# Optimization experiments

Measured on AMD Instinct MI355X. Metric: run time of the kernel, lower is better.

## Reference

```python
import jax, jax.numpy as jnp
import numpy as np

B, S = 8, 8192        # batch of texts, chars per text
D = 64                # char_emb_size = (64, 64)
V = 96                # len(valid_chars) + 1


def setup_inputs() -> dict:
    key = jax.random.key(0)
    k_ids, k_emb = jax.random.split(key)
    # tokenized text: indices into valid_chars (always < V-1, matching .index())
    text_ids = jax.random.randint(k_ids, (B, S), 0, V - 1).astype(jnp.int32)
    # frozen embedding table, row i -> flattened D x D matrix
    emb = jax.random.normal(k_emb, (V, D * D), dtype=jnp.float32)
    return {"text_ids": text_ids, "emb": emb}


def reference(text_ids, emb):
    b, s = text_ids.shape
    d = int(np.sqrt(emb.shape[1]))
    table = emb.reshape(-1, d, d)                      # [V, D, D]
    # context_vec starts as identity (torch.eye(max(emb_size)))
    ctx0 = jnp.broadcast_to(jnp.eye(d, dtype=emb.dtype), (b, d, d))

    def step(ctx, ids_t):
        # ids_t: [B] char ids at this timestep
        E = table[ids_t]                               # [B, D, D] gather
        ctx = jnp.cos(jnp.einsum('bij,bjk->bik', ctx, E))
        return ctx, None

    ctx, _ = jax.lax.scan(step, ctx0, text_ids.T)      # scan over S
    return ctx                                         # [B, D, D]
```

## Files before the change

kernel.cpp:

```cpp
#include <hip/hip_runtime.h>


#define BB 8
#define SS 8192
#define DD 64

__device__ __forceinline__ float host_cosf(float y)
{
#pragma clang fp contract(off)
    const double hpi_inv = 0x1.45F306DC9C883p+23;
    const double hpi     = 0x1.921FB54442D18p0;
    const double c0 = 0x1p0;
    const double c1 = -0x1.ffffffd0c621cp-2;
    const double c2 = 0x1.55553e1068f19p-5;
    const double c3 = -0x1.6c087e89a359dp-10;
    const double c4 = 0x1.99343027bf8c3p-16;
    const double s1 = -0x1.555545995a603p-3;
    const double s2 = 0x1.1107605230bc4p-7;
    const double s3 = -0x1.994eb3774cf24p-13;

    const double x = (double)y;
    double r  = x * hpi_inv;
    int    n  = (((int)r) + 0x800000) >> 24;
    double xr = fma(-(double)n, hpi, x);

    const int  mm   = (n + 1) & 3;
    const double s  = (mm == 1 || mm == 2) ? -1.0 : 1.0;
    const bool negt = (mm & 2) != 0;

    double x2  = xr * xr;
    double x4  = x2 * x2;
    double cc2 = fma(x2, c4, c3);
    double cc1 = fma(x2, c1, c0);
    double x6  = x4 * x2;
    double cp  = fma(x4, c2, cc1);
    float fcos = (float)fma(x6, cc2, cp);
    fcos = negt ? -fcos : fcos;

    double xs  = xr * s;
    double x3  = xs * x2;
    double sp1 = fma(x2, s3, s2);
    double x7  = x3 * x2;
    double sr  = fma(x3, s1, xs);
    float fsin = (float)fma(x7, sp1, sr);

    return (n & 1) ? fsin : fcos;
}

__global__ void transpose_kernel(const float* __restrict__ emb,
                                 float* __restrict__ embT)
{
    const int id = blockIdx.x;
    const int t  = threadIdx.x;
    const float* src = emb + (size_t)id * (DD * DD);
    float*       dst = embT + (size_t)id * (DD * DD);
#pragma unroll
    for (int kk = 0; kk < 16; ++kk) {
        const int lin = kk * 256 + t;
        const int j = lin >> 6, c = lin & 63;
        dst[(j >> 2) * 256 + c * 4 + (j & 3)] = src[lin];
    }
}

#define ROX(S,J)   "v_readlane_b32 s" #S ", %[vr], " #J "\n\t"
#define FRX(S,E,J) "v_fmac_f32 %[acc], s" #S ", v" #E "\n\t" \
                   "v_readlane_b32 s" #S ", %[vr], " #J "\n\t"
#define FOX(S,E)   "v_fmac_f32 %[acc], s" #S ", v" #E "\n\t"
#define WQ         "s_waitcnt vmcnt(15)\n\t"
#define LDQ(D0,D3,VO,OFF) \
    "global_load_dwordx4 v[" #D0 ":" #D3 "], " VO ", s[46:47] offset:" OFF "\n\t"

__global__ __launch_bounds__(64, 1)
void text2vec_kernel(const int* __restrict__ ids,
                     const float* __restrict__ emb,
                     const float* __restrict__ embT,
                     float* __restrict__ out)
{
    const int blk  = blockIdx.x;
    const int b    = blk & 7;
    const int r    = blk >> 3;
    const int lane = threadIdx.x;

    const int* bids = ids + b * SS;
    const uintptr_t ta = (uintptr_t)embT;
    const unsigned tlo = (unsigned)ta, thi = (unsigned)(ta >> 32);
    unsigned vo0 = (unsigned)lane * 16u;
    unsigned vo1 = vo0 + 4096u, vo2 = vo0 + 8192u, vo3 = vo0 + 12288u;

    const int id0 = bids[0], id1 = bids[1], id2 = bids[2];

    float acc  = emb[(size_t)(unsigned)id0 * (DD * DD) + r * DD + lane];
    float vrow = 0.0f;

    const double d_hpinv = 0x1.45F306DC9C883p+23;
    const double d_hpi   = 0x1.921FB54442D18p0;
    const double d_c0 = 0x1p0;
    const double d_c1 = -0x1.ffffffd0c621cp-2;
    const double d_c2 = 0x1.55553e1068f19p-5;
    const double d_c3 = -0x1.6c087e89a359dp-10;
    const double d_c4 = 0x1.99343027bf8c3p-16;
    const double d_s1 = -0x1.555545995a603p-3;
    const double d_s2 = 0x1.1107605230bc4p-7;
    const double d_s3 = -0x1.994eb3774cf24p-13;

    asm volatile(
        "s_lshl_b32 s44, %[id1], 14\n\t"
        "s_add_u32 s46, %[tlo], s44\n\t"
        "s_addc_u32 s47, %[thi], 0\n\t"
        LDQ(64,67,"%[vo0]","0")    LDQ(68,71,"%[vo0]","1024")
        LDQ(72,75,"%[vo0]","2048") LDQ(76,79,"%[vo0]","3072")
        LDQ(80,83,"%[vo1]","0")    LDQ(84,87,"%[vo1]","1024")
        LDQ(88,91,"%[vo1]","2048") LDQ(92,95,"%[vo1]","3072")
        LDQ(96,99,"%[vo2]","0")    LDQ(100,103,"%[vo2]","1024")
        LDQ(104,107,"%[vo2]","2048") LDQ(108,111,"%[vo2]","3072")
        LDQ(112,115,"%[vo3]","0")  LDQ(116,119,"%[vo3]","1024")
        LDQ(120,123,"%[vo3]","2048") LDQ(124,127,"%[vo3]","3072")
        "s_mov_b32 s41, %[id2]\n\t"
        "s_mov_b32 s40, 1\n\t"

        "T2V_LOOP:\n\t"
        "v_cvt_f64_f32 v[8:9], %[acc]\n\t"
        "v_mul_f64 v[10:11], v[8:9], %[hpinv]\n\t"
        "v_cvt_i32_f64 v12, v[10:11]\n\t"
        "v_add_u32 v12, 0x800000, v12\n\t"
        "v_ashrrev_i32 v12, 24, v12\n\t"
        "v_cvt_f64_i32 v[10:11], v12\n\t"
        "v_fma_f64 v[8:9], -v[10:11], %[hpi], v[8:9]\n\t"
        "v_add_u32 v13, 1, v12\n\t"
        "v_and_b32 v14, 2, v13\n\t"
        "v_cmp_ne_u32 s[56:57], 0, v14\n\t"
        "v_and_b32 v14, 3, v13\n\t"
        "v_add_u32 v14, 1, v14\n\t"
        "v_and_b32 v14, 2, v14\n\t"
        "v_cmp_ne_u32 vcc, 0, v14\n\t"
        "v_mov_b32 v14, 0x3ff00000\n\t"
        "v_mov_b32 v15, 0xbff00000\n\t"
        "v_cndmask_b32 v15, v14, v15, vcc\n\t"
        "v_mov_b32 v14, 0\n\t"
        "v_mul_f64 v[16:17], v[8:9], v[8:9]\n\t"
        "v_mul_f64 v[18:19], v[16:17], v[16:17]\n\t"
        "v_fma_f64 v[20:21], v[16:17], %[c4], %[c3]\n\t"
        "v_fma_f64 v[22:23], v[16:17], %[c1], %[c0]\n\t"
        "v_mul_f64 v[24:25], v[18:19], v[16:17]\n\t"
        "v_fma_f64 v[22:23], v[18:19], %[c2], v[22:23]\n\t"
        "v_fma_f64 v[20:21], v[24:25], v[20:21], v[22:23]\n\t"
        "v_cvt_f32_f64 v26, v[20:21]\n\t"
        "v_xor_b32 v27, 0x80000000, v26\n\t"
        "v_cndmask_b32 v26, v26, v27, s[56:57]\n\t"
        "v_mul_f64 v[18:19], v[8:9], v[14:15]\n\t"
        "v_mul_f64 v[20:21], v[18:19], v[16:17]\n\t"
        "v_fma_f64 v[22:23], v[16:17], %[s3], %[s2]\n\t"
        "v_mul_f64 v[24:25], v[20:21], v[16:17]\n\t"
        "v_fma_f64 v[18:19], v[20:21], %[s1], v[18:19]\n\t"
        "v_fma_f64 v[18:19], v[24:25], v[22:23], v[18:19]\n\t"
        "v_cvt_f32_f64 v27, v[18:19]\n\t"
        "v_and_b32 v14, 1, v12\n\t"
        "v_cmp_ne_u32 vcc, 0, v14\n\t"
        "v_cndmask_b32 %[vr], v26, v27, vcc\n\t"
        "v_mov_b32 %[acc], 0\n\t"
        "s_waitcnt lgkmcnt(0)\n\t"
        "s_lshl_b32 s44, s41, 14\n\t"
        "s_add_u32 s46, %[tlo], s44\n\t"
        "s_addc_u32 s47, %[thi], 0\n\t"
        "s_add_u32 s43, s40, 2\n\t"
        "s_and_b32 s43, s43, 8191\n\t"
        "s_lshl_b32 s43, s43, 2\n\t"
        "s_load_dword s41, %[bids], s43\n\t"
        ROX(50,0) ROX(51,1) ROX(52,2) ROX(53,3) ROX(54,4) ROX(55,5)
        WQ FRX(50,64,6)   FRX(51,65,7)   FRX(52,66,8)   FRX(53,67,9)   LDQ(64,67,"%[vo0]","0")
        WQ FRX(54,68,10)  FRX(55,69,11)  FRX(50,70,12)  FRX(51,71,13)  LDQ(68,71,"%[vo0]","1024")
        WQ FRX(52,72,14)  FRX(53,73,15)  FRX(54,74,16)  FRX(55,75,17)  LDQ(72,75,"%[vo0]","2048")
        WQ FRX(50,76,18)  FRX(51,77,19)  FRX(52,78,20)  FRX(53,79,21)  LDQ(76,79,"%[vo0]","3072")
        WQ FRX(54,80,22)  FRX(55,81,23)  FRX(50,82,24)  FRX(51,83,25)  LDQ(80,83,"%[vo1]","0")
        WQ FRX(52,84,26)  FRX(53,85,27)  FRX(54,86,28)  FRX(55,87,29)  LDQ(84,87,"%[vo1]","1024")
        WQ FRX(50,88,30)  FRX(51,89,31)  FRX(52,90,32)  FRX(53,91,33)  LDQ(88,91,"%[vo1]","2048")
        WQ FRX(54,92,34)  FRX(55,93,35)  FRX(50,94,36)  FRX(51,95,37)  LDQ(92,95,"%[vo1]","3072")
        WQ FRX(52,96,38)  FRX(53,97,39)  FRX(54,98,40)  FRX(55,99,41)  LDQ(96,99,"%[vo2]","0")
        WQ FRX(50,100,42) FRX(51,101,43) FRX(52,102,44) FRX(53,103,45) LDQ(100,103,"%[vo2]","1024")
        WQ FRX(54,104,46) FRX(55,105,47) FRX(50,106,48) FRX(51,107,49) LDQ(104,107,"%[vo2]","2048")
        WQ FRX(52,108,50) FRX(53,109,51) FRX(54,110,52) FRX(55,111,53) LDQ(108,111,"%[vo2]","3072")
        WQ FRX(50,112,54) FRX(51,113,55) FRX(52,114,56) FRX(53,115,57) LDQ(112,115,"%[vo3]","0")
        WQ FRX(54,116,58) FRX(55,117,59) FRX(50,118,60) FRX(51,119,61) LDQ(116,119,"%[vo3]","1024")
        WQ FRX(52,120,62) FRX(53,121,63) FOX(54,122)    FOX(55,123)    LDQ(120,123,"%[vo3]","2048")
        WQ FOX(50,124)    FOX(51,125)    FOX(52,126)    FOX(53,127)    LDQ(124,127,"%[vo3]","3072")
        "s_addk_i32 s40, 1\n\t"
        "s_cmpk_lt_i32 s40, 0x2000\n\t"
        "s_cbranch_scc1 T2V_LOOP\n\t"
        "s_waitcnt vmcnt(0) lgkmcnt(0)\n\t"
        : [acc] "+v"(acc), [vr] "+v"(vrow)
        : [tlo] "s"(tlo), [thi] "s"(thi), [bids] "s"(bids),
          [vo0] "v"(vo0), [vo1] "v"(vo1), [vo2] "v"(vo2), [vo3] "v"(vo3),
          [id1] "s"(id1), [id2] "s"(id2),
          [hpinv] "s"(d_hpinv), [hpi] "s"(d_hpi), [c4] "s"(d_c4),
          [c1] "s"(d_c1), [c2] "s"(d_c2), [s1] "s"(d_s1), [s3] "s"(d_s3),
          [c3] "v"(d_c3), [c0] "v"(d_c0), [s2] "v"(d_s2)
        : "memory", "scc", "vcc",
          "s40","s41","s42","s43","s44","s45","s46","s47",
          "s50","s51","s52","s53","s54","s55","s56","s57",
          "v8","v9","v10","v11","v12","v13","v14","v15","v16","v17",
          "v18","v19","v20","v21","v22","v23","v24","v25","v26","v27",
          "v64","v65","v66","v67","v68","v69","v70","v71",
          "v72","v73","v74","v75","v76","v77","v78","v79",
          "v80","v81","v82","v83","v84","v85","v86","v87",
          "v88","v89","v90","v91","v92","v93","v94","v95",
          "v96","v97","v98","v99","v100","v101","v102","v103",
          "v104","v105","v106","v107","v108","v109","v110","v111",
          "v112","v113","v114","v115","v116","v117","v118","v119",
          "v120","v121","v122","v123","v124","v125","v126","v127");

    vrow = host_cosf(acc);
    out[b * (DD * DD) + r * DD + lane] = vrow;
}

extern "C" void kernel_launch(void* const* d_in, const int* in_sizes, int n_in,
                              void* d_out, int out_size, void* d_ws, size_t ws_size,
                              hipStream_t stream)
{
    const int*   ids = (const int*)  d_in[0];
    const float* emb = (const float*)d_in[1];
    float*       out = (float*)      d_out;
    float*       embT = (float*)     d_ws;

    const int V = in_sizes[1] / (DD * DD);

    transpose_kernel<<<dim3(V), dim3(256), 0, stream>>>(emb, embT);
    text2vec_kernel<<<dim3(BB * DD), dim3(DD), 0, stream>>>(ids, emb, embT, out);
}
```

Measured before the change: 3.708 ms.

## Compute two context rows per wavefront to reuse each streamed embedding load

Each 64-lane block now owns two rows of the context matrix instead of one. Every embedding-matrix column it streams from global memory feeds two FMA chains, and the two cosine evaluations are interleaved for ILP. The grid is halved, so block count and global/L2 load traffic per step both drop. The cost is more serial VALU and readlane work per wave on a latency-bound recurrence, fewer waves to spread across CUs, and more clobbered SGPRs.

```diff
diff --git a/kernel.cpp b/kernel.cpp
--- a/kernel.cpp
+++ b/kernel.cpp
@@ -62,10 +62,12 @@
     }
 }
 
-#define ROX(S,J)   "v_readlane_b32 s" #S ", %[vr], " #J "\n\t"
-#define FRX(S,E,J) "v_fmac_f32 %[acc], s" #S ", v" #E "\n\t" \
-                   "v_readlane_b32 s" #S ", %[vr], " #J "\n\t"
-#define FOX(S,E)   "v_fmac_f32 %[acc], s" #S ", v" #E "\n\t"
+#define RLA(S,J)   "v_readlane_b32 s" #S ", %[vra], " #J "\n\t"
+#define RLB(S,J)   "v_readlane_b32 s" #S ", %[vrb], " #J "\n\t"
+#define FMA_(S,E)  "v_fmac_f32 %[aca], s" #S ", v" #E "\n\t"
+#define FMB_(S,E)  "v_fmac_f32 %[acb], s" #S ", v" #E "\n\t"
+#define DSLOT(SA,SB,E,J)  FMA_(SA,E) FMB_(SB,E) RLA(SA,J) RLB(SB,J)
+#define DSLOTN(SA,SB,E)   FMA_(SA,E) FMB_(SB,E)
 #define WQ         "s_waitcnt vmcnt(15)\n\t"
 #define LDQ(D0,D3,VO,OFF) \
     "global_load_dwordx4 v[" #D0 ":" #D3 "], " VO ", s[46:47] offset:" OFF "\n\t"
@@ -78,7 +80,8 @@
 {
     const int blk  = blockIdx.x;
     const int b    = blk & 7;
-    const int r    = blk >> 3;
+    const int rp   = blk >> 3;
+    const int r0   = rp * 2, r1 = rp * 2 + 1;
     const int lane = threadIdx.x;
 
     const int* bids = ids + b * SS;
@@ -89,8 +92,9 @@
 
     const int id0 = bids[0], id1 = bids[1], id2 = bids[2];
 
-    float acc  = emb[(size_t)(unsigned)id0 * (DD * DD) + r * DD + lane];
-    float vrow = 0.0f;
+    float aca = emb[(size_t)(unsigned)id0 * (DD * DD) + r0 * DD + lane];
+    float acb = emb[(size_t)(unsigned)id0 * (DD * DD) + r1 * DD + lane];
+    float vra = 0.0f, vrb = 0.0f;
 
     const double d_hpinv = 0x1.45F306DC9C883p+23;
     const double d_hpi   = 0x1.921FB54442D18p0;
@@ -119,45 +123,84 @@
         "s_mov_b32 s40, 1\n\t"
 
         "T2V_LOOP:\n\t"
-        "v_cvt_f64_f32 v[8:9], %[acc]\n\t"
+        "v_cvt_f64_f32 v[8:9], %[aca]\n\t"
+        "v_cvt_f64_f32 v[28:29], %[acb]\n\t"
         "v_mul_f64 v[10:11], v[8:9], %[hpinv]\n\t"
+        "v_mul_f64 v[30:31], v[28:29], %[hpinv]\n\t"
         "v_cvt_i32_f64 v12, v[10:11]\n\t"
+        "v_cvt_i32_f64 v32, v[30:31]\n\t"
         "v_add_u32 v12, 0x800000, v12\n\t"
+        "v_add_u32 v32, 0x800000, v32\n\t"
         "v_ashrrev_i32 v12, 24, v12\n\t"
+        "v_ashrrev_i32 v32, 24, v32\n\t"
         "v_cvt_f64_i32 v[10:11], v12\n\t"
+        "v_cvt_f64_i32 v[30:31], v32\n\t"
         "v_fma_f64 v[8:9], -v[10:11], %[hpi], v[8:9]\n\t"
+        "v_fma_f64 v[28:29], -v[30:31], %[hpi], v[28:29]\n\t"
         "v_add_u32 v13, 1, v12\n\t"
+        "v_add_u32 v33, 1, v32\n\t"
         "v_and_b32 v14, 2, v13\n\t"
+        "v_and_b32 v34, 2, v33\n\t"
         "v_cmp_ne_u32 s[56:57], 0, v14\n\t"
+        "v_cmp_ne_u32 s[58:59], 0, v34\n\t"
         "v_and_b32 v14, 3, v13\n\t"
+        "v_and_b32 v34, 3, v33\n\t"
         "v_add_u32 v14, 1, v14\n\t"
+        "v_add_u32 v34, 1, v34\n\t"
         "v_and_b32 v14, 2, v14\n\t"
-        "v_cmp_ne_u32 vcc, 0, v14\n\t"
+        "v_and_b32 v34, 2, v34\n\t"
+        "v_cmp_ne_u32 s[36:37], 0, v14\n\t"
+        "v_cmp_ne_u32 s[38:39], 0, v34\n\t"
         "v_mov_b32 v14, 0x3ff00000\n\t"
         "v_mov_b32 v15, 0xbff00000\n\t"
-        "v_cndmask_b32 v15, v14, v15, vcc\n\t"
+        "v_cndmask_b32 v15, v14, v15, s[36:37]\n\t"
+        "v_mov_b32 v34, 0x3ff00000\n\t"
+        "v_mov_b32 v35, 0xbff00000\n\t"
+        "v_cndmask_b32 v35, v34, v35, s[38:39]\n\t"
         "v_mov_b32 v14, 0\n\t"
+        "v_mov_b32 v34, 0\n\t"
         "v_mul_f64 v[16:17], v[8:9], v[8:9]\n\t"
+        "v_mul_f64 v[36:37], v[28:29], v[28:29]\n\t"
         "v_mul_f64 v[18:19], v[16:17], v[16:17]\n\t"
+        "v_mul_f64 v[38:39], v[36:37], v[36:37]\n\t"
         "v_fma_f64 v[20:21], v[16:17], %[c4], %[c3]\n\t"
+        "v_fma_f64 v[40:41], v[36:37], %[c4], %[c3]\n\t"
         "v_fma_f64 v[22:23], v[16:17], %[c1], %[c0]\n\t"
+        "v_fma_f64 v[42:43], v[36:37], %[c1], %[c0]\n\t"
         "v_mul_f64 v[24:25], v[18:19], v[16:17]\n\t"
+        "v_mul_f64 v[44:45], v[38:39], v[36:37]\n\t"
         "v_fma_f64 v[22:23], v[18:19], %[c2], v[22:23]\n\t"
+        "v_fma_f64 v[42:43], v[38:39], %[c2], v[42:43]\n\t"
         "v_fma_f64 v[20:21], v[24:25], v[20:21], v[22:23]\n\t"
+        "v_fma_f64 v[40:41], v[44:45], v[40:41], v[42:43]\n\t"
         "v_cvt_f32_f64 v26, v[20:21]\n\t"
+        "v_cvt_f32_f64 v46, v[40:41]\n\t"
         "v_xor_b32 v27, 0x80000000, v26\n\t"
+        "v_xor_b32 v47, 0x80000000, v46\n\t"
         "v_cndmask_b32 v26, v26, v27, s[56:57]\n\t"
+        "v_cndmask_b32 v46, v46, v47, s[58:59]\n\t"
         "v_mul_f64 v[18:19], v[8:9], v[14:15]\n\t"
+        "v_mul_f64 v[38:39], v[28:29], v[34:35]\n\t"
         "v_mul_f64 v[20:21], v[18:19], v[16:17]\n\t"
+        "v_mul_f64 v[40:41], v[38:39], v[36:37]\n\t"
         "v_fma_f64 v[22:23], v[16:17], %[s3], %[s2]\n\t"
+        "v_fma_f64 v[42:43], v[36:37], %[s3], %[s2]\n\t"
         "v_mul_f64 v[24:25], v[20:21], v[16:17]\n\t"
+        "v_mul_f64 v[44:45], v[40:41], v[36:37]\n\t"
         "v_fma_f64 v[18:19], v[20:21], %[s1], v[18:19]\n\t"
+        "v_fma_f64 v[38:39], v[40:41], %[s1], v[38:39]\n\t"
         "v_fma_f64 v[18:19], v[24:25], v[22:23], v[18:19]\n\t"
+        "v_fma_f64 v[38:39], v[44:45], v[42:43], v[38:39]\n\t"
         "v_cvt_f32_f64 v27, v[18:19]\n\t"
+        "v_cvt_f32_f64 v47, v[38:39]\n\t"
         "v_and_b32 v14, 1, v12\n\t"
-        "v_cmp_ne_u32 vcc, 0, v14\n\t"
-        "v_cndmask_b32 %[vr], v26, v27, vcc\n\t"
-        "v_mov_b32 %[acc], 0\n\t"
+        "v_and_b32 v34, 1, v32\n\t"
+        "v_cmp_ne_u32 s[30:31], 0, v14\n\t"
+        "v_cmp_ne_u32 s[32:33], 0, v34\n\t"
+        "v_cndmask_b32 %[vra], v26, v27, s[30:31]\n\t"
+        "v_cndmask_b32 %[vrb], v46, v47, s[32:33]\n\t"
+        "v_mov_b32 %[aca], 0\n\t"
+        "v_mov_b32 %[acb], 0\n\t"
         "s_waitcnt lgkmcnt(0)\n\t"
         "s_lshl_b32 s44, s41, 14\n\t"
         "s_add_u32 s46, %[tlo], s44\n\t"
@@ -166,28 +209,29 @@
         "s_and_b32 s43, s43, 8191\n\t"
         "s_lshl_b32 s43, s43, 2\n\t"
         "s_load_dword s41, %[bids], s43\n\t"
-        ROX(50,0) ROX(51,1) ROX(52,2) ROX(53,3) ROX(54,4) ROX(55,5)
-        WQ FRX(50,64,6)   FRX(51,65,7)   FRX(52,66,8)   FRX(53,67,9)   LDQ(64,67,"%[vo0]","0")
-        WQ FRX(54,68,10)  FRX(55,69,11)  FRX(50,70,12)  FRX(51,71,13)  LDQ(68,71,"%[vo0]","1024")
-        WQ FRX(52,72,14)  FRX(53,73,15)  FRX(54,74,16)  FRX(55,75,17)  LDQ(72,75,"%[vo0]","2048")
-        WQ FRX(50,76,18)  FRX(51,77,19)  FRX(52,78,20)  FRX(53,79,21)  LDQ(76,79,"%[vo0]","3072")
-        WQ FRX(54,80,22)  FRX(55,81,23)  FRX(50,82,24)  FRX(51,83,25)  LDQ(80,83,"%[vo1]","0")
-        WQ FRX(52,84,26)  FRX(53,85,27)  FRX(54,86,28)  FRX(55,87,29)  LDQ(84,87,"%[vo1]","1024")
-        WQ FRX(50,88,30)  FRX(51,89,31)  FRX(52,90,32)  FRX(53,91,33)  LDQ(88,91,"%[vo1]","2048")
-        WQ FRX(54,92,34)  FRX(55,93,35)  FRX(50,94,36)  FRX(51,95,37)  LDQ(92,95,"%[vo1]","3072")
-        WQ FRX(52,96,38)  FRX(53,97,39)  FRX(54,98,40)  FRX(55,99,41)  LDQ(96,99,"%[vo2]","0")
-        WQ FRX(50,100,42) FRX(51,101,43) FRX(52,102,44) FRX(53,103,45) LDQ(100,103,"%[vo2]","1024")
-        WQ FRX(54,104,46) FRX(55,105,47) FRX(50,106,48) FRX(51,107,49) LDQ(104,107,"%[vo2]","2048")
-        WQ FRX(52,108,50) FRX(53,109,51) FRX(54,110,52) FRX(55,111,53) LDQ(108,111,"%[vo2]","3072")
-        WQ FRX(50,112,54) FRX(51,113,55) FRX(52,114,56) FRX(53,115,57) LDQ(112,115,"%[vo3]","0")
-        WQ FRX(54,116,58) FRX(55,117,59) FRX(50,118,60) FRX(51,119,61) LDQ(116,119,"%[vo3]","1024")
-        WQ FRX(52,120,62) FRX(53,121,63) FOX(54,122)    FOX(55,123)    LDQ(120,123,"%[vo3]","2048")
-        WQ FOX(50,124)    FOX(51,125)    FOX(52,126)    FOX(53,127)    LDQ(124,127,"%[vo3]","3072")
+        RLA(50,0) RLB(60,0) RLA(51,1) RLB(61,1) RLA(52,2) RLB(62,2)
+        RLA(53,3) RLB(63,3) RLA(54,4) RLB(64,4) RLA(55,5) RLB(65,5)
+        WQ DSLOT(50,60,64,6)   DSLOT(51,61,65,7)   DSLOT(52,62,66,8)   DSLOT(53,63,67,9)   LDQ(64,67,"%[vo0]","0")
+        WQ DSLOT(54,64,68,10)  DSLOT(55,65,69,11)  DSLOT(50,60,70,12)  DSLOT(51,61,71,13)  LDQ(68,71,"%[vo0]","1024")
+        WQ DSLOT(52,62,72,14)  DSLOT(53,63,73,15)  DSLOT(54,64,74,16)  DSLOT(55,65,75,17)  LDQ(72,75,"%[vo0]","2048")
+        WQ DSLOT(50,60,76,18)  DSLOT(51,61,77,19)  DSLOT(52,62,78,20)  DSLOT(53,63,79,21)  LDQ(76,79,"%[vo0]","3072")
+        WQ DSLOT(54,64,80,22)  DSLOT(55,65,81,23)  DSLOT(50,60,82,24)  DSLOT(51,61,83,25)  LDQ(80,83,"%[vo1]","0")
+        WQ DSLOT(52,62,84,26)  DSLOT(53,63,85,27)  DSLOT(54,64,86,28)  DSLOT(55,65,87,29)  LDQ(84,87,"%[vo1]","1024")
+        WQ DSLOT(50,60,88,30)  DSLOT(51,61,89,31)  DSLOT(52,62,90,32)  DSLOT(53,63,91,33)  LDQ(88,91,"%[vo1]","2048")
+        WQ DSLOT(54,64,92,34)  DSLOT(55,65,93,35)  DSLOT(50,60,94,36)  DSLOT(51,61,95,37)  LDQ(92,95,"%[vo1]","3072")
+        WQ DSLOT(52,62,96,38)  DSLOT(53,63,97,39)  DSLOT(54,64,98,40)  DSLOT(55,65,99,41)  LDQ(96,99,"%[vo2]","0")
+        WQ DSLOT(50,60,100,42) DSLOT(51,61,101,43) DSLOT(52,62,102,44) DSLOT(53,63,103,45) LDQ(100,103,"%[vo2]","1024")
+        WQ DSLOT(54,64,104,46) DSLOT(55,65,105,47) DSLOT(50,60,106,48) DSLOT(51,61,107,49) LDQ(104,107,"%[vo2]","2048")
+        WQ DSLOT(52,62,108,50) DSLOT(53,63,109,51) DSLOT(54,64,110,52) DSLOT(55,65,111,53) LDQ(108,111,"%[vo2]","3072")
+        WQ DSLOT(50,60,112,54) DSLOT(51,61,113,55) DSLOT(52,62,114,56) DSLOT(53,63,115,57) LDQ(112,115,"%[vo3]","0")
+        WQ DSLOT(54,64,116,58) DSLOT(55,65,117,59) DSLOT(50,60,118,60) DSLOT(51,61,119,61) LDQ(116,119,"%[vo3]","1024")
+        WQ DSLOT(52,62,120,62) DSLOT(53,63,121,63) DSLOTN(54,64,122)   DSLOTN(55,65,123)   LDQ(120,123,"%[vo3]","2048")
+        WQ DSLOTN(50,60,124)   DSLOTN(51,61,125)   DSLOTN(52,62,126)   DSLOTN(53,63,127)   LDQ(124,127,"%[vo3]","3072")
         "s_addk_i32 s40, 1\n\t"
         "s_cmpk_lt_i32 s40, 0x2000\n\t"
         "s_cbranch_scc1 T2V_LOOP\n\t"
         "s_waitcnt vmcnt(0) lgkmcnt(0)\n\t"
-        : [acc] "+v"(acc), [vr] "+v"(vrow)
+        : [aca] "+v"(aca), [acb] "+v"(acb), [vra] "+v"(vra), [vrb] "+v"(vrb)
         : [tlo] "s"(tlo), [thi] "s"(thi), [bids] "s"(bids),
           [vo0] "v"(vo0), [vo1] "v"(vo1), [vo2] "v"(vo2), [vo3] "v"(vo3),
           [id1] "s"(id1), [id2] "s"(id2),
@@ -195,10 +239,14 @@
           [c1] "s"(d_c1), [c2] "s"(d_c2), [s1] "s"(d_s1), [s3] "s"(d_s3),
           [c3] "v"(d_c3), [c0] "v"(d_c0), [s2] "v"(d_s2)
         : "memory", "scc", "vcc",
+          "s30","s31","s32","s33","s36","s37","s38","s39",
           "s40","s41","s42","s43","s44","s45","s46","s47",
-          "s50","s51","s52","s53","s54","s55","s56","s57",
+          "s50","s51","s52","s53","s54","s55","s56","s57","s58","s59",
+          "s60","s61","s62","s63","s64","s65",
           "v8","v9","v10","v11","v12","v13","v14","v15","v16","v17",
           "v18","v19","v20","v21","v22","v23","v24","v25","v26","v27",
+          "v28","v29","v30","v31","v32","v33","v34","v35","v36","v37",
+          "v38","v39","v40","v41","v42","v43","v44","v45","v46","v47",
           "v64","v65","v66","v67","v68","v69","v70","v71",
           "v72","v73","v74","v75","v76","v77","v78","v79",
           "v80","v81","v82","v83","v84","v85","v86","v87",
@@ -208,8 +256,10 @@
           "v112","v113","v114","v115","v116","v117","v118","v119",
           "v120","v121","v122","v123","v124","v125","v126","v127");
 
-    vrow = host_cosf(acc);
-    out[b * (DD * DD) + r * DD + lane] = vrow;
+    vra = host_cosf(aca);
+    vrb = host_cosf(acb);
+    out[b * (DD * DD) + r0 * DD + lane] = vra;
+    out[b * (DD * DD) + r1 * DD + lane] = vrb;
 }
 
 extern "C" void kernel_launch(void* const* d_in, const int* in_sizes, int n_in,
@@ -224,5 +274,5 @@
     const int V = in_sizes[1] / (DD * DD);
 
     transpose_kernel<<<dim3(V), dim3(256), 0, stream>>>(emb, embT);
-    text2vec_kernel<<<dim3(BB * DD), dim3(DD), 0, stream>>>(ids, emb, embT, out);
-}
+    text2vec_kernel<<<dim3(BB * DD / 2), dim3(DD), 0, stream>>>(ids, emb, embT, out);
+}
```

Result: slower. 5.773 ms (+55.7%).

## Double-buffer embedding row loads across two register sets in scan loop

Applied to the files above, without the earlier changes.

Replaces the single 64-register load buffer, which was refilled piecemeal inside the FMA chain with per-quad waits, by two alternating register sets (v64-127 and v160-223). The loop is unrolled by two: the next step's matrix slice is prefetched into the idle set while the cosine is computed, and the FMA chain then runs on the other set without interleaved loads. This aims to hide global load latency behind the cosine and FMA work and to remove the waitcnt stalls inside the chain, at the cost of many more VGPRs and a separate epilogue iteration.

```diff
diff --git a/kernel.cpp b/kernel.cpp
--- a/kernel.cpp
+++ b/kernel.cpp
@@ -62,13 +62,118 @@
     }
 }
 
-#define ROX(S,J)   "v_readlane_b32 s" #S ", %[vr], " #J "\n\t"
+#define ROX(S,J)   "v_readlane_b32 s" #S ", %[vra], " #J "\n\t"
 #define FRX(S,E,J) "v_fmac_f32 %[acc], s" #S ", v" #E "\n\t" \
-                   "v_readlane_b32 s" #S ", %[vr], " #J "\n\t"
+                   "v_readlane_b32 s" #S ", %[vra], " #J "\n\t"
 #define FOX(S,E)   "v_fmac_f32 %[acc], s" #S ", v" #E "\n\t"
-#define WQ         "s_waitcnt vmcnt(15)\n\t"
-#define LDQ(D0,D3,VO,OFF) \
+#define GLD(D0,D3,VO,OFF) \
     "global_load_dwordx4 v[" #D0 ":" #D3 "], " VO ", s[46:47] offset:" OFF "\n\t"
+
+#define GLDA_Q0 GLD(64,67,"%[vo0]","0")    GLD(68,71,"%[vo0]","1024") \
+                GLD(72,75,"%[vo0]","2048") GLD(76,79,"%[vo0]","3072")
+#define GLDA_Q1 GLD(80,83,"%[vo1]","0")    GLD(84,87,"%[vo1]","1024") \
+                GLD(88,91,"%[vo1]","2048") GLD(92,95,"%[vo1]","3072")
+#define GLDA_Q2 GLD(96,99,"%[vo2]","0")    GLD(100,103,"%[vo2]","1024") \
+                GLD(104,107,"%[vo2]","2048") GLD(108,111,"%[vo2]","3072")
+#define GLDA_Q3 GLD(112,115,"%[vo3]","0")  GLD(116,119,"%[vo3]","1024") \
+                GLD(120,123,"%[vo3]","2048") GLD(124,127,"%[vo3]","3072")
+#define GLDB_Q0 GLD(160,163,"%[vo0]","0")    GLD(164,167,"%[vo0]","1024") \
+                GLD(168,171,"%[vo0]","2048") GLD(172,175,"%[vo0]","3072")
+#define GLDB_Q1 GLD(176,179,"%[vo1]","0")    GLD(180,183,"%[vo1]","1024") \
+                GLD(184,187,"%[vo1]","2048") GLD(188,191,"%[vo1]","3072")
+#define GLDB_Q2 GLD(192,195,"%[vo2]","0")    GLD(196,199,"%[vo2]","1024") \
+                GLD(200,203,"%[vo2]","2048") GLD(204,207,"%[vo2]","3072")
+#define GLDB_Q3 GLD(208,211,"%[vo3]","0")    GLD(212,215,"%[vo3]","1024") \
+                GLD(216,219,"%[vo3]","2048") GLD(220,223,"%[vo3]","3072")
+
+#define COS_A "v_cvt_f64_f32 v[8:9], %[acc]\n\t"
+#define COS_B "v_mul_f64 v[10:11], v[8:9], %[hpinv]\n\t" \
+              "v_cvt_i32_f64 v12, v[10:11]\n\t" \
+              "v_add_u32 v12, 0x800000, v12\n\t" \
+              "v_ashrrev_i32 v12, 24, v12\n\t" \
+              "v_cvt_f64_i32 v[10:11], v12\n\t" \
+              "v_fma_f64 v[8:9], -v[10:11], %[hpi], v[8:9]\n\t"
+#define COS_C "v_add_u32 v13, 1, v12\n\t" \
+              "v_and_b32 v14, 2, v13\n\t" \
+              "v_cmp_ne_u32 s[56:57], 0, v14\n\t" \
+              "v_and_b32 v14, 3, v13\n\t" \
+              "v_add_u32 v14, 1, v14\n\t" \
+              "v_and_b32 v14, 2, v14\n\t" \
+              "v_cmp_ne_u32 vcc, 0, v14\n\t" \
+              "v_mov_b32 v14, 0x3ff00000\n\t" \
+              "v_mov_b32 v15, 0xbff00000\n\t" \
+              "v_cndmask_b32 v15, v14, v15, vcc\n\t" \
+              "v_mov_b32 v14, 0\n\t"
+#define COS_D "v_mul_f64 v[16:17], v[8:9], v[8:9]\n\t" \
+              "v_mul_f64 v[18:19], v[16:17], v[16:17]\n\t" \
+              "v_fma_f64 v[20:21], v[16:17], %[c4], %[c3]\n\t" \
+              "v_fma_f64 v[22:23], v[16:17], %[c1], %[c0]\n\t" \
+              "v_mul_f64 v[24:25], v[18:19], v[16:17]\n\t" \
+              "v_fma_f64 v[22:23], v[18:19], %[c2], v[22:23]\n\t" \
+              "v_fma_f64 v[20:21], v[24:25], v[20:21], v[22:23]\n\t" \
+              "v_cvt_f32_f64 v26, v[20:21]\n\t" \
+              "v_xor_b32 v27, 0x80000000, v26\n\t" \
+              "v_cndmask_b32 v26, v26, v27, s[56:57]\n\t"
+#define COS_E "v_mul_f64 v[18:19], v[8:9], v[14:15]\n\t" \
+              "v_mul_f64 v[20:21], v[18:19], v[16:17]\n\t" \
+              "v_fma_f64 v[22:23], v[16:17], %[s3], %[s2]\n\t" \
+              "v_mul_f64 v[24:25], v[20:21], v[16:17]\n\t" \
+              "v_fma_f64 v[18:19], v[20:21], %[s1], v[18:19]\n\t" \
+              "v_fma_f64 v[18:19], v[24:25], v[22:23], v[18:19]\n\t" \
+              "v_cvt_f32_f64 v27, v[18:19]\n\t" \
+              "v_and_b32 v14, 1, v12\n\t" \
+              "v_cmp_ne_u32 vcc, 0, v14\n\t" \
+              "v_cndmask_b32 %[vra], v26, v27, vcc\n\t" \
+              "v_mov_b32 %[acc], 0\n\t"
+
+#define BASECALC \
+    "s_waitcnt lgkmcnt(0)\n\t" \
+    "s_lshl_b32 s44, s41, 14\n\t" \
+    "s_add_u32 s46, %[tlo], s44\n\t" \
+    "s_addc_u32 s47, %[thi], 0\n\t"
+#define IDLOAD \
+    "s_add_u32 s43, s40, 2\n\t" \
+    "s_and_b32 s43, s43, 8191\n\t" \
+    "s_lshl_b32 s43, s43, 2\n\t" \
+    "s_load_dword s41, %[bids], s43\n\t"
+
+#define CHAIN_A \
+    ROX(50,0) ROX(51,1) ROX(52,2) ROX(53,3) ROX(54,4) ROX(55,5) \
+    FRX(50,64,6)   FRX(51,65,7)   FRX(52,66,8)   FRX(53,67,9) \
+    FRX(54,68,10)  FRX(55,69,11)  FRX(50,70,12)  FRX(51,71,13) \
+    FRX(52,72,14)  FRX(53,73,15)  FRX(54,74,16)  FRX(55,75,17) \
+    FRX(50,76,18)  FRX(51,77,19)  FRX(52,78,20)  FRX(53,79,21) \
+    FRX(54,80,22)  FRX(55,81,23)  FRX(50,82,24)  FRX(51,83,25) \
+    FRX(52,84,26)  FRX(53,85,27)  FRX(54,86,28)  FRX(55,87,29) \
+    FRX(50,88,30)  FRX(51,89,31)  FRX(52,90,32)  FRX(53,91,33) \
+    FRX(54,92,34)  FRX(55,93,35)  FRX(50,94,36)  FRX(51,95,37) \
+    FRX(52,96,38)  FRX(53,97,39)  FRX(54,98,40)  FRX(55,99,41) \
+    FRX(50,100,42) FRX(51,101,43) FRX(52,102,44) FRX(53,103,45) \
+    FRX(54,104,46) FRX(55,105,47) FRX(50,106,48) FRX(51,107,49) \
+    FRX(52,108,50) FRX(53,109,51) FRX(54,110,52) FRX(55,111,53) \
+    FRX(50,112,54) FRX(51,113,55) FRX(52,114,56) FRX(53,115,57) \
+    FRX(54,116,58) FRX(55,117,59) FRX(50,118,60) FRX(51,119,61) \
+    FRX(52,120,62) FRX(53,121,63) FOX(54,122)    FOX(55,123) \
+    FOX(50,124)    FOX(51,125)    FOX(52,126)    FOX(53,127)
+
+#define CHAIN_B \
+    ROX(50,0) ROX(51,1) ROX(52,2) ROX(53,3) ROX(54,4) ROX(55,5) \
+    FRX(50,160,6)   FRX(51,161,7)   FRX(52,162,8)   FRX(53,163,9) \
+    FRX(54,164,10)  FRX(55,165,11)  FRX(50,166,12)  FRX(51,167,13) \
+    FRX(52,168,14)  FRX(53,169,15)  FRX(54,170,16)  FRX(55,171,17) \
+    FRX(50,172,18)  FRX(51,173,19)  FRX(52,174,20)  FRX(53,175,21) \
+    FRX(54,176,22)  FRX(55,177,23)  FRX(50,178,24)  FRX(51,179,25) \
+    FRX(52,180,26)  FRX(53,181,27)  FRX(54,182,28)  FRX(55,183,29) \
+    FRX(50,184,30)  FRX(51,185,31)  FRX(52,186,32)  FRX(53,187,33) \
+    FRX(54,188,34)  FRX(55,189,35)  FRX(50,190,36)  FRX(51,191,37) \
+    FRX(52,192,38)  FRX(53,193,39)  FRX(54,194,40)  FRX(55,195,41) \
+    FRX(50,196,42)  FRX(51,197,43)  FRX(52,198,44)  FRX(53,199,45) \
+    FRX(54,200,46)  FRX(55,201,47)  FRX(50,202,48)  FRX(51,203,49) \
+    FRX(52,204,50)  FRX(53,205,51)  FRX(54,206,52)  FRX(55,207,53) \
+    FRX(50,208,54)  FRX(51,209,55)  FRX(52,210,56)  FRX(53,211,57) \
+    FRX(54,212,58)  FRX(55,213,59)  FRX(50,214,60)  FRX(51,215,61) \
+    FRX(52,216,62)  FRX(53,217,63)  FOX(54,218)     FOX(55,219) \
+    FOX(50,220)     FOX(51,221)     FOX(52,222)     FOX(53,223)
 
 __global__ __launch_bounds__(64, 1)
 void text2vec_kernel(const int* __restrict__ ids,
@@ -90,7 +195,7 @@
     const int id0 = bids[0], id1 = bids[1], id2 = bids[2];
 
     float acc  = emb[(size_t)(unsigned)id0 * (DD * DD) + r * DD + lane];
-    float vrow = 0.0f;
+    float vra  = 0.0f;
 
     const double d_hpinv = 0x1.45F306DC9C883p+23;
     const double d_hpi   = 0x1.921FB54442D18p0;
@@ -107,87 +212,39 @@
         "s_lshl_b32 s44, %[id1], 14\n\t"
         "s_add_u32 s46, %[tlo], s44\n\t"
         "s_addc_u32 s47, %[thi], 0\n\t"
-        LDQ(64,67,"%[vo0]","0")    LDQ(68,71,"%[vo0]","1024")
-        LDQ(72,75,"%[vo0]","2048") LDQ(76,79,"%[vo0]","3072")
-        LDQ(80,83,"%[vo1]","0")    LDQ(84,87,"%[vo1]","1024")
-        LDQ(88,91,"%[vo1]","2048") LDQ(92,95,"%[vo1]","3072")
-        LDQ(96,99,"%[vo2]","0")    LDQ(100,103,"%[vo2]","1024")
-        LDQ(104,107,"%[vo2]","2048") LDQ(108,111,"%[vo2]","3072")
-        LDQ(112,115,"%[vo3]","0")  LDQ(116,119,"%[vo3]","1024")
-        LDQ(120,123,"%[vo3]","2048") LDQ(124,127,"%[vo3]","3072")
+        GLDA_Q0 GLDA_Q1 GLDA_Q2 GLDA_Q3
         "s_mov_b32 s41, %[id2]\n\t"
         "s_mov_b32 s40, 1\n\t"
 
         "T2V_LOOP:\n\t"
-        "v_cvt_f64_f32 v[8:9], %[acc]\n\t"
-        "v_mul_f64 v[10:11], v[8:9], %[hpinv]\n\t"
-        "v_cvt_i32_f64 v12, v[10:11]\n\t"
-        "v_add_u32 v12, 0x800000, v12\n\t"
-        "v_ashrrev_i32 v12, 24, v12\n\t"
-        "v_cvt_f64_i32 v[10:11], v12\n\t"
-        "v_fma_f64 v[8:9], -v[10:11], %[hpi], v[8:9]\n\t"
-        "v_add_u32 v13, 1, v12\n\t"
-        "v_and_b32 v14, 2, v13\n\t"
-        "v_cmp_ne_u32 s[56:57], 0, v14\n\t"
-        "v_and_b32 v14, 3, v13\n\t"
-        "v_add_u32 v14, 1, v14\n\t"
-        "v_and_b32 v14, 2, v14\n\t"
-        "v_cmp_ne_u32 vcc, 0, v14\n\t"
-        "v_mov_b32 v14, 0x3ff00000\n\t"
-        "v_mov_b32 v15, 0xbff00000\n\t"
-        "v_cndmask_b32 v15, v14, v15, vcc\n\t"
-        "v_mov_b32 v14, 0\n\t"
-        "v_mul_f64 v[16:17], v[8:9], v[8:9]\n\t"
-        "v_mul_f64 v[18:19], v[16:17], v[16:17]\n\t"
-        "v_fma_f64 v[20:21], v[16:17], %[c4], %[c3]\n\t"
-        "v_fma_f64 v[22:23], v[16:17], %[c1], %[c0]\n\t"
-        "v_mul_f64 v[24:25], v[18:19], v[16:17]\n\t"
-        "v_fma_f64 v[22:23], v[18:19], %[c2], v[22:23]\n\t"
-        "v_fma_f64 v[20:21], v[24:25], v[20:21], v[22:23]\n\t"
-        "v_cvt_f32_f64 v26, v[20:21]\n\t"
-        "v_xor_b32 v27, 0x80000000, v26\n\t"
-        "v_cndmask_b32 v26, v26, v27, s[56:57]\n\t"
-        "v_mul_f64 v[18:19], v[8:9], v[14:15]\n\t"
-        "v_mul_f64 v[20:21], v[18:19], v[16:17]\n\t"
-        "v_fma_f64 v[22:23], v[16:17], %[s3], %[s2]\n\t"
-        "v_mul_f64 v[24:25], v[20:21], v[16:17]\n\t"
-        "v_fma_f64 v[18:19], v[20:21], %[s1], v[18:19]\n\t"
-        "v_fma_f64 v[18:19], v[24:25], v[22:23], v[18:19]\n\t"
-        "v_cvt_f32_f64 v27, v[18:19]\n\t"
-        "v_and_b32 v14, 1, v12\n\t"
-        "v_cmp_ne_u32 vcc, 0, v14\n\t"
-        "v_cndmask_b32 %[vr], v26, v27, vcc\n\t"
-        "v_mov_b32 %[acc], 0\n\t"
+        BASECALC
+        COS_A GLDB_Q0
+        COS_B GLDB_Q1
+        COS_C GLDB_Q2
+        COS_D GLDB_Q3
+        IDLOAD
+        COS_E
+        "s_waitcnt vmcnt(16)\n\t"
+        CHAIN_A
+        "s_addk_i32 s40, 1\n\t"
+        BASECALC
+        COS_A GLDA_Q0
+        COS_B GLDA_Q1
+        COS_C GLDA_Q2
+        COS_D GLDA_Q3
+        IDLOAD
+        COS_E
+        "s_waitcnt vmcnt(16)\n\t"
+        CHAIN_B
+        "s_addk_i32 s40, 1\n\t"
+        "s_cmpk_lt_i32 s40, 0x1FFF\n\t"
+        "s_cbranch_scc1 T2V_LOOP\n\t"
         "s_waitcnt lgkmcnt(0)\n\t"
-        "s_lshl_b32 s44, s41, 14\n\t"
-        "s_add_u32 s46, %[tlo], s44\n\t"
-        "s_addc_u32 s47, %[thi], 0\n\t"
-        "s_add_u32 s43, s40, 2\n\t"
-        "s_and_b32 s43, s43, 8191\n\t"
-        "s_lshl_b32 s43, s43, 2\n\t"
-        "s_load_dword s41, %[bids], s43\n\t"
-        ROX(50,0) ROX(51,1) ROX(52,2) ROX(53,3) ROX(54,4) ROX(55,5)
-        WQ FRX(50,64,6)   FRX(51,65,7)   FRX(52,66,8)   FRX(53,67,9)   LDQ(64,67,"%[vo0]","0")
-        WQ FRX(54,68,10)  FRX(55,69,11)  FRX(50,70,12)  FRX(51,71,13)  LDQ(68,71,"%[vo0]","1024")
-        WQ FRX(52,72,14)  FRX(53,73,15)  FRX(54,74,16)  FRX(55,75,17)  LDQ(72,75,"%[vo0]","2048")
-        WQ FRX(50,76,18)  FRX(51,77,19)  FRX(52,78,20)  FRX(53,79,21)  LDQ(76,79,"%[vo0]","3072")
-        WQ FRX(54,80,22)  FRX(55,81,23)  FRX(50,82,24)  FRX(51,83,25)  LDQ(80,83,"%[vo1]","0")
-        WQ FRX(52,84,26)  FRX(53,85,27)  FRX(54,86,28)  FRX(55,87,29)  LDQ(84,87,"%[vo1]","1024")
-        WQ FRX(50,88,30)  FRX(51,89,31)  FRX(52,90,32)  FRX(53,91,33)  LDQ(88,91,"%[vo1]","2048")
-        WQ FRX(54,92,34)  FRX(55,93,35)  FRX(50,94,36)  FRX(51,95,37)  LDQ(92,95,"%[vo1]","3072")
-        WQ FRX(52,96,38)  FRX(53,97,39)  FRX(54,98,40)  FRX(55,99,41)  LDQ(96,99,"%[vo2]","0")
-        WQ FRX(50,100,42) FRX(51,101,43) FRX(52,102,44) FRX(53,103,45) LDQ(100,103,"%[vo2]","1024")
-        WQ FRX(54,104,46) FRX(55,105,47) FRX(50,106,48) FRX(51,107,49) LDQ(104,107,"%[vo2]","2048")
-        WQ FRX(52,108,50) FRX(53,109,51) FRX(54,110,52) FRX(55,111,53) LDQ(108,111,"%[vo2]","3072")
-        WQ FRX(50,112,54) FRX(51,113,55) FRX(52,114,56) FRX(53,115,57) LDQ(112,115,"%[vo3]","0")
-        WQ FRX(54,116,58) FRX(55,117,59) FRX(50,118,60) FRX(51,119,61) LDQ(116,119,"%[vo3]","1024")
-        WQ FRX(52,120,62) FRX(53,121,63) FOX(54,122)    FOX(55,123)    LDQ(120,123,"%[vo3]","2048")
-        WQ FOX(50,124)    FOX(51,125)    FOX(52,126)    FOX(53,127)    LDQ(124,127,"%[vo3]","3072")
-        "s_addk_i32 s40, 1\n\t"
-        "s_cmpk_lt_i32 s40, 0x2000\n\t"
-        "s_cbranch_scc1 T2V_LOOP\n\t"
+        COS_A COS_B COS_C COS_D COS_E
+        "s_waitcnt vmcnt(0)\n\t"
+        CHAIN_A
         "s_waitcnt vmcnt(0) lgkmcnt(0)\n\t"
-        : [acc] "+v"(acc), [vr] "+v"(vrow)
+        : [acc] "+v"(acc), [vra] "+v"(vra)
         : [tlo] "s"(tlo), [thi] "s"(thi), [bids] "s"(bids),
           [vo0] "v"(vo0), [vo1] "v"(vo1), [vo2] "v"(vo2), [vo3] "v"(vo3),
           [id1] "s"(id1), [id2] "s"(id2),
@@ -206,10 +263,18 @@
           "v96","v97","v98","v99","v100","v101","v102","v103",
           "v104","v105","v106","v107","v108","v109","v110","v111",
           "v112","v113","v114","v115","v116","v117","v118","v119",
-          "v120","v121","v122","v123","v124","v125","v126","v127");
-
-    vrow = host_cosf(acc);
-    out[b * (DD * DD) + r * DD + lane] = vrow;
+          "v120","v121","v122","v123","v124","v125","v126","v127",
+          "v160","v161","v162","v163","v164","v165","v166","v167",
+          "v168","v169","v170","v171","v172","v173","v174","v175",
+          "v176","v177","v178","v179","v180","v181","v182","v183",
+          "v184","v185","v186","v187","v188","v189","v190","v191",
+          "v192","v193","v194","v195","v196","v197","v198","v199",
+          "v200","v201","v202","v203","v204","v205","v206","v207",
+          "v208","v209","v210","v211","v212","v213","v214","v215",
+          "v216","v217","v218","v219","v220","v221","v222","v223");
+
+    vra = host_cosf(acc);
+    out[b * (DD * DD) + r * DD + lane] = vra;
 }
 
 extern "C" void kernel_launch(void* const* d_in, const int* in_sizes, int n_in,
```

Measured after the change: 3.111 ms. -16.1%, faster.
